# Optimization experiments

Measured on AMD Instinct MI355X. Metric: run time of the kernel, lower is better.

The kernel has to match this reference:

```python
import jax, jax.numpy as jnp
import numpy as np


def setup_inputs() -> dict:
    key = jax.random.key(0)
    k1, _ = jax.random.split(key)
    N, H, CH, T = 4, 8, 64, 2048
    qkv = jax.random.normal(k1, (N, H * 3 * CH, T), dtype=jnp.float32)
    rescale = jnp.ones((1,), dtype=jnp.float32)
    return {"qkv": qkv, "rescale": rescale, "n_heads": H}


def reference(qkv, rescale, n_heads):
    bs, width, length = qkv.shape
    ch = width // (3 * n_heads)
    # [N, H*3*C, T] -> [N*H, 3*C, T] -> three [N*H, C, T]
    qkv_h = qkv.reshape(bs * n_heads, 3 * ch, length)
    q, k, v = qkv_h[:, :ch], qkv_h[:, ch:2 * ch], qkv_h[:, 2 * ch:]
    scale = 1.0 / jnp.sqrt(jnp.sqrt(jnp.float32(ch)))
    # scores: [B*H, T, S]
    weight = jnp.einsum('bct,bcs->bts', q * scale, k * scale)
    weight = jax.nn.softmax(weight.astype(jnp.float32) * rescale[0], axis=-1).astype(qkv.dtype)
    a = jnp.einsum('bts,bcs->bct', weight, v)  # [B*H, C, T]
    return a.reshape(bs, n_heads * ch, length)
```

## Files before the change

### kernel.cpp

```cpp
#include <hip/hip_runtime.h>
#include <stdint.h>

typedef _Float16 half8 __attribute__((ext_vector_type(8)));
typedef _Float16 half4 __attribute__((ext_vector_type(4)));
typedef __fp16   fp16x2 __attribute__((ext_vector_type(2)));
typedef float    floatx4 __attribute__((ext_vector_type(4)));

#define T_LEN 2048
#define CH 64
#define BH 32
#define QTILE 64
#define LDP 72
#define PTP 72
#define FRAG_BH 131072

__global__ __launch_bounds__(256, 2)
void prep_kernel(const float* __restrict__ qkv, const float* __restrict__ rescale,
                 _Float16* __restrict__ ws)
{
    __shared__ _Float16 Qs[64][LDP];
    __shared__ _Float16 Ks[64][LDP];
    __shared__ _Float16 Vs[64][LDP];

    const int tid  = threadIdx.x;
    const int bh   = blockIdx.y;
    const int tile = blockIdx.x;
    const int x0   = tile * 64;

    const float qscale = 0.125f * 1.4426950408889634f * rescale[0];

    const float* qp = qkv + (size_t)(bh >> 3) * (1536 * T_LEN)
                          + (size_t)(bh & 7) * (192 * T_LEN);
    const float* kp = qp + 64 * T_LEN;
    const float* vp = qp + 128 * T_LEN;

    {
        const int a4 = (tid & 15) * 4;
        const int c4 = (tid >> 4) * 4;
        float4 rq[4], rk[4];
#pragma unroll
        for (int i = 0; i < 4; ++i) {
            rq[i] = *(const float4*)(qp + (size_t)(c4 + i) * T_LEN + x0 + a4);
            rk[i] = *(const float4*)(kp + (size_t)(c4 + i) * T_LEN + x0 + a4);
        }
#pragma unroll
        for (int j = 0; j < 4; ++j) {
            half4 hq, hk;
#pragma unroll
            for (int i = 0; i < 4; ++i) {
                hq[i] = (_Float16)((&rq[i].x)[j] * qscale);
                hk[i] = (_Float16)((&rk[i].x)[j]);
            }
            *(half4*)&Qs[a4 + j][c4] = hq;
            *(half4*)&Ks[a4 + j][c4] = hk;
        }
        const int s4 = (tid & 15) * 4;
        const int cv = tid >> 4;
#pragma unroll
        for (int i = 0; i < 4; ++i) {
            const int c = cv + 16 * i;
            float4 r = *(const float4*)(vp + (size_t)c * T_LEN + x0 + s4);
            half4 h; h[0]=(_Float16)r.x; h[1]=(_Float16)r.y; h[2]=(_Float16)r.z; h[3]=(_Float16)r.w;
            *(half4*)&Vs[c][s4] = h;
        }
    }
    __syncthreads();

    const int lane = tid & 63, wave = tid >> 6;
    const int l15 = lane & 15, quad = lane >> 4;
    _Float16* qf = ws;
    _Float16* kf = ws + (size_t)BH * FRAG_BH;
    _Float16* vf = ws + (size_t)2 * BH * FRAG_BH;

#pragma unroll
    for (int ks = 0; ks < 2; ++ks) {
        half8 hq = *(const half8*)&Qs[wave * 16 + l15][ks * 32 + quad * 8];
        half8 hk = *(const half8*)&Ks[wave * 16 + l15][ks * 32 + quad * 8];
        half8 hv = *(const half8*)&Vs[wave * 16 + l15][ks * 32 + quad * 8];
        const size_t gqk = (((size_t)bh * 128 + tile * 4 + wave) * 2 + ks) * 512 + lane * 8;
        *(half8*)(qf + gqk) = hq;
        *(half8*)(kf + gqk) = hk;
        *(half8*)(vf + (((size_t)bh * 32 + tile) * 8 + wave * 2 + ks) * 512 + lane * 8) = hv;
    }
}

__global__ __launch_bounds__(256, 4)
void attn_kernel(const _Float16* __restrict__ ws, float* __restrict__ out)
{
    __shared__ _Float16 Pt[4][16][PTP];

    const int tid  = threadIdx.x;
    const int wave = tid >> 6;
    const int lane = tid & 63;
    const int l15  = lane & 15;
    const int quad = lane >> 4;

    const int bid  = blockIdx.x;
    const int xcd  = bid & 7;
    const int slot = bid >> 3;
    const int bh   = (slot & 3) * 8 + xcd;
    const int tile = slot >> 2;
    const int t0   = tile * QTILE;

    const _Float16* qf = ws;
    const _Float16* kf = ws + (size_t)BH * FRAG_BH;
    const _Float16* vf = ws + (size_t)2 * BH * FRAG_BH;
    float* op = out + (size_t)bh * (CH * T_LEN);

    const _Float16* kfp = kf + (size_t)bh * FRAG_BH + lane * 8;
    const _Float16* vfp = vf + (size_t)bh * FRAG_BH + lane * 8;

    half8 bq[2];
#pragma unroll
    for (int ks = 0; ks < 2; ++ks)
        bq[ks] = *(const half8*)(qf +
            (((size_t)bh * 128 + tile * 4 + wave) * 2 + ks) * 512 + lane * 8);

    const floatx4 fzero = {0.f, 0.f, 0.f, 0.f};
    floatx4 oacc[4];
#pragma unroll
    for (int ct = 0; ct < 4; ++ct) oacc[ct] = fzero;
    floatx4 lacc = fzero;

    half8 bones;
#pragma unroll
    for (int i = 0; i < 8; ++i) bones[i] = (_Float16)1.0f;

    half8 ak[4][2];
    half8 bv[4][2];
    half8 ap[2];

    auto do_qk_exp = [&]() {
        floatx4 sacc[4];
#pragma unroll
        for (int mt = 0; mt < 4; ++mt) sacc[mt] = fzero;
#pragma unroll
        for (int mt = 0; mt < 4; ++mt)
#pragma unroll
            for (int ks = 0; ks < 2; ++ks)
                sacc[mt] = __builtin_amdgcn_mfma_f32_16x16x32_f16(
                    ak[mt][ks], bq[ks], sacc[mt], 0, 0, 0);

#pragma unroll
        for (int mt = 0; mt < 4; ++mt) {
            fp16x2 p01 = __builtin_amdgcn_cvt_pkrtz(
                __builtin_amdgcn_exp2f(sacc[mt][0]),
                __builtin_amdgcn_exp2f(sacc[mt][1]));
            fp16x2 p23 = __builtin_amdgcn_cvt_pkrtz(
                __builtin_amdgcn_exp2f(sacc[mt][2]),
                __builtin_amdgcn_exp2f(sacc[mt][3]));
            half4 ph;
            ph[0] = (_Float16)p01[0]; ph[1] = (_Float16)p01[1];
            ph[2] = (_Float16)p23[0]; ph[3] = (_Float16)p23[1];
            *(half4*)&Pt[wave][l15][mt * 16 + quad * 4] = ph;
        }
#pragma unroll
        for (int ks = 0; ks < 2; ++ks)
            ap[ks] = *(const half8*)&Pt[wave][l15][ks * 32 + quad * 8];
    };

#pragma unroll
    for (int mt = 0; mt < 4; ++mt)
#pragma unroll
        for (int ks = 0; ks < 2; ++ks)
            ak[mt][ks] = *(const half8*)(kfp + (size_t)(mt * 2 + ks) * 512);
#pragma unroll
    for (int ct = 0; ct < 4; ++ct)
#pragma unroll
        for (int ks = 0; ks < 2; ++ks)
            bv[ct][ks] = *(const half8*)(vfp + (size_t)(ct * 2 + ks) * 512);
    do_qk_exp();
#pragma unroll
    for (int mt = 0; mt < 4; ++mt)
#pragma unroll
        for (int ks = 0; ks < 2; ++ks)
            ak[mt][ks] = *(const half8*)(kfp + 4096 + (size_t)(mt * 2 + ks) * 512);

#pragma unroll 2
    for (int st = 1; st < 32; ++st) {
#pragma unroll
        for (int ks = 0; ks < 2; ++ks)
            lacc = __builtin_amdgcn_mfma_f32_16x16x32_f16(ap[ks], bones, lacc, 0, 0, 0);
#pragma unroll
        for (int ct = 0; ct < 4; ++ct)
#pragma unroll
            for (int ks = 0; ks < 2; ++ks)
                oacc[ct] = __builtin_amdgcn_mfma_f32_16x16x32_f16(
                    ap[ks], bv[ct][ks], oacc[ct], 0, 0, 0);

        const _Float16* vcur = vfp + (size_t)st * 4096;
#pragma unroll
        for (int ct = 0; ct < 4; ++ct)
#pragma unroll
            for (int ks = 0; ks < 2; ++ks)
                bv[ct][ks] = *(const half8*)(vcur + (size_t)(ct * 2 + ks) * 512);

        do_qk_exp();

        if (st < 31) {
            const _Float16* kcur = kfp + (size_t)(st + 1) * 4096;
#pragma unroll
            for (int mt = 0; mt < 4; ++mt)
#pragma unroll
                for (int ks = 0; ks < 2; ++ks)
                    ak[mt][ks] = *(const half8*)(kcur + (size_t)(mt * 2 + ks) * 512);
        }
    }

#pragma unroll
    for (int ks = 0; ks < 2; ++ks)
        lacc = __builtin_amdgcn_mfma_f32_16x16x32_f16(ap[ks], bones, lacc, 0, 0, 0);
#pragma unroll
    for (int ct = 0; ct < 4; ++ct)
#pragma unroll
        for (int ks = 0; ks < 2; ++ks)
            oacc[ct] = __builtin_amdgcn_mfma_f32_16x16x32_f16(
                ap[ks], bv[ct][ks], oacc[ct], 0, 0, 0);

    {
        float linv[4];
#pragma unroll
        for (int r = 0; r < 4; ++r) linv[r] = 1.0f / lacc[r];
#pragma unroll
        for (int ct = 0; ct < 4; ++ct) {
            const int c = ct * 16 + l15;
            const int t = t0 + wave * 16 + quad * 4;
            float4 o;
#pragma unroll
            for (int r = 0; r < 4; ++r)
                (&o.x)[r] = oacc[ct][r] * linv[r];
            *(float4*)(op + (size_t)c * T_LEN + t) = o;
        }
    }
}

extern "C" void kernel_launch(void* const* d_in, const int* in_sizes, int n_in,
                              void* d_out, int out_size, void* d_ws, size_t ws_size,
                              hipStream_t stream) {
    const float* qkv     = (const float*)d_in[0];
    const float* rescale = (const float*)d_in[1];
    float* out = (float*)d_out;
    _Float16* ws = (_Float16*)d_ws;

    prep_kernel<<<dim3(32, BH), dim3(256), 0, stream>>>(qkv, rescale, ws);
    attn_kernel<<<dim3(T_LEN / QTILE * BH), dim3(256), 0, stream>>>(ws, out);
}
```

Before: 153.5 us.

## Split key range across waves, keep P in registers, reduce partial outputs via LDS

The attention kernel now gives each wave a quarter of the key positions for all 64 queries in the tile, instead of a separate 16-query slice. Score-tile exponentials are fed straight into 16x16x16 MFMAs as the B operand, which removes the LDS round-trip for P. Row sums are accumulated in scalar registers rather than through ones-MFMAs, and V is stored in a new fragment layout that matches the new operand shape. The price is a cross-wave reduction of the partial outputs through LDS with several barriers, more accumulator registers (occupancy lowered to 3 blocks), and twice as many smaller MFMAs for the PV product.

```diff
diff --git a/kernel.cpp b/kernel.cpp
--- a/kernel.cpp
+++ b/kernel.cpp
@@ -5,13 +5,13 @@
 typedef _Float16 half4 __attribute__((ext_vector_type(4)));
 typedef __fp16   fp16x2 __attribute__((ext_vector_type(2)));
 typedef float    floatx4 __attribute__((ext_vector_type(4)));
+typedef unsigned uintx2 __attribute__((ext_vector_type(2)));
 
 #define T_LEN 2048
 #define CH 64
 #define BH 32
 #define QTILE 64
 #define LDP 72
-#define PTP 72
 #define FRAG_BH 131072
 
 __global__ __launch_bounds__(256, 2)
@@ -76,18 +76,24 @@
     for (int ks = 0; ks < 2; ++ks) {
         half8 hq = *(const half8*)&Qs[wave * 16 + l15][ks * 32 + quad * 8];
         half8 hk = *(const half8*)&Ks[wave * 16 + l15][ks * 32 + quad * 8];
-        half8 hv = *(const half8*)&Vs[wave * 16 + l15][ks * 32 + quad * 8];
         const size_t gqk = (((size_t)bh * 128 + tile * 4 + wave) * 2 + ks) * 512 + lane * 8;
         *(half8*)(qf + gqk) = hq;
         *(half8*)(kf + gqk) = hk;
-        *(half8*)(vf + (((size_t)bh * 32 + tile) * 8 + wave * 2 + ks) * 512 + lane * 8) = hv;
+    }
+#pragma unroll
+    for (int ct = 0; ct < 4; ++ct) {
+        half4 hv = *(const half4*)&Vs[ct * 16 + l15][wave * 16 + quad * 4];
+        *(half4*)(vf + (size_t)bh * FRAG_BH
+                     + ((size_t)(tile * 4 + wave) * 4 + ct) * 256 + lane * 4) = hv;
     }
 }
 
-__global__ __launch_bounds__(256, 4)
+__global__ __launch_bounds__(256, 3)
 void attn_kernel(const _Float16* __restrict__ ws, float* __restrict__ out)
 {
-    __shared__ _Float16 Pt[4][16][PTP];
+    __shared__ float Os[4][64][16];
+    __shared__ float Lred[4][64];
+    __shared__ float Lfin[64];
 
     const int tid  = threadIdx.x;
     const int wave = tid >> 6;
@@ -107,129 +113,104 @@
     const _Float16* vf = ws + (size_t)2 * BH * FRAG_BH;
     float* op = out + (size_t)bh * (CH * T_LEN);
 
-    const _Float16* kfp = kf + (size_t)bh * FRAG_BH + lane * 8;
-    const _Float16* vfp = vf + (size_t)bh * FRAG_BH + lane * 8;
-
-    half8 bq[2];
-#pragma unroll
-    for (int ks = 0; ks < 2; ++ks)
-        bq[ks] = *(const half8*)(qf +
-            (((size_t)bh * 128 + tile * 4 + wave) * 2 + ks) * 512 + lane * 8);
+    const _Float16* kfp = kf + (size_t)bh * FRAG_BH + wave * 1024 + lane * 8;
+    const _Float16* vfp = vf + (size_t)bh * FRAG_BH + wave * 1024 + lane * 4;
+
+    half8 bq[4][2];
+#pragma unroll
+    for (int tt = 0; tt < 4; ++tt)
+#pragma unroll
+        for (int ks = 0; ks < 2; ++ks)
+            bq[tt][ks] = *(const half8*)(qf +
+                (((size_t)bh * 128 + tile * 4 + tt) * 2 + ks) * 512 + lane * 8);
 
     const floatx4 fzero = {0.f, 0.f, 0.f, 0.f};
-    floatx4 oacc[4];
-#pragma unroll
-    for (int ct = 0; ct < 4; ++ct) oacc[ct] = fzero;
-    floatx4 lacc = fzero;
-
-    half8 bones;
-#pragma unroll
-    for (int i = 0; i < 8; ++i) bones[i] = (_Float16)1.0f;
-
-    half8 ak[4][2];
-    half8 bv[4][2];
-    half8 ap[2];
-
-    auto do_qk_exp = [&]() {
-        floatx4 sacc[4];
-#pragma unroll
-        for (int mt = 0; mt < 4; ++mt) sacc[mt] = fzero;
-#pragma unroll
-        for (int mt = 0; mt < 4; ++mt)
+    floatx4 oacc[4][4];
+#pragma unroll
+    for (int ct = 0; ct < 4; ++ct)
+#pragma unroll
+        for (int tt = 0; tt < 4; ++tt) oacc[ct][tt] = fzero;
+    float lsum[4] = {0.f, 0.f, 0.f, 0.f};
+
+    half8 akA[2], akB[2];
+    half4 bvA[4], bvB[4];
+
+    auto load_kv = [&](half8 (&ak)[2], half4 (&bv)[4], int st) {
+        const _Float16* kp = kfp + (size_t)st * 4096;
+        ak[0] = *(const half8*)kp;
+        ak[1] = *(const half8*)(kp + 512);
+        const _Float16* vp = vfp + (size_t)st * 4096;
+#pragma unroll
+        for (int ct = 0; ct < 4; ++ct)
+            bv[ct] = *(const half4*)(vp + ct * 256);
+    };
+
+    auto body = [&](half8 (&akC)[2], half4 (&bvC)[4],
+                    half8 (&akN)[2], half4 (&bvN)[4], int st) {
+        if (st < 31) load_kv(akN, bvN, st + 1);
+#pragma unroll
+        for (int tt = 0; tt < 4; ++tt) {
+            floatx4 sacc = fzero;
 #pragma unroll
             for (int ks = 0; ks < 2; ++ks)
-                sacc[mt] = __builtin_amdgcn_mfma_f32_16x16x32_f16(
-                    ak[mt][ks], bq[ks], sacc[mt], 0, 0, 0);
-
-#pragma unroll
-        for (int mt = 0; mt < 4; ++mt) {
-            fp16x2 p01 = __builtin_amdgcn_cvt_pkrtz(
-                __builtin_amdgcn_exp2f(sacc[mt][0]),
-                __builtin_amdgcn_exp2f(sacc[mt][1]));
-            fp16x2 p23 = __builtin_amdgcn_cvt_pkrtz(
-                __builtin_amdgcn_exp2f(sacc[mt][2]),
-                __builtin_amdgcn_exp2f(sacc[mt][3]));
-            half4 ph;
-            ph[0] = (_Float16)p01[0]; ph[1] = (_Float16)p01[1];
-            ph[2] = (_Float16)p23[0]; ph[3] = (_Float16)p23[1];
-            *(half4*)&Pt[wave][l15][mt * 16 + quad * 4] = ph;
-        }
-#pragma unroll
-        for (int ks = 0; ks < 2; ++ks)
-            ap[ks] = *(const half8*)&Pt[wave][l15][ks * 32 + quad * 8];
+                sacc = __builtin_amdgcn_mfma_f32_16x16x32_f16(
+                    akC[ks], bq[tt][ks], sacc, 0, 0, 0);
+            float e0 = __builtin_amdgcn_exp2f(sacc[0]);
+            float e1 = __builtin_amdgcn_exp2f(sacc[1]);
+            float e2 = __builtin_amdgcn_exp2f(sacc[2]);
+            float e3 = __builtin_amdgcn_exp2f(sacc[3]);
+            lsum[tt] += (e0 + e1) + (e2 + e3);
+            fp16x2 p01 = __builtin_amdgcn_cvt_pkrtz(e0, e1);
+            fp16x2 p23 = __builtin_amdgcn_cvt_pkrtz(e2, e3);
+            uintx2 uu;
+            uu[0] = __builtin_bit_cast(unsigned, p01);
+            uu[1] = __builtin_bit_cast(unsigned, p23);
+            half4 pb = __builtin_bit_cast(half4, uu);
+#pragma unroll
+            for (int ct = 0; ct < 4; ++ct)
+                oacc[ct][tt] = __builtin_amdgcn_mfma_f32_16x16x16f16(
+                    bvC[ct], pb, oacc[ct][tt], 0, 0, 0);
+        }
     };
 
-#pragma unroll
-    for (int mt = 0; mt < 4; ++mt)
-#pragma unroll
-        for (int ks = 0; ks < 2; ++ks)
-            ak[mt][ks] = *(const half8*)(kfp + (size_t)(mt * 2 + ks) * 512);
-#pragma unroll
-    for (int ct = 0; ct < 4; ++ct)
-#pragma unroll
-        for (int ks = 0; ks < 2; ++ks)
-            bv[ct][ks] = *(const half8*)(vfp + (size_t)(ct * 2 + ks) * 512);
-    do_qk_exp();
-#pragma unroll
-    for (int mt = 0; mt < 4; ++mt)
-#pragma unroll
-        for (int ks = 0; ks < 2; ++ks)
-            ak[mt][ks] = *(const half8*)(kfp + 4096 + (size_t)(mt * 2 + ks) * 512);
-
-#pragma unroll 2
-    for (int st = 1; st < 32; ++st) {
-#pragma unroll
-        for (int ks = 0; ks < 2; ++ks)
-            lacc = __builtin_amdgcn_mfma_f32_16x16x32_f16(ap[ks], bones, lacc, 0, 0, 0);
-#pragma unroll
-        for (int ct = 0; ct < 4; ++ct)
-#pragma unroll
-            for (int ks = 0; ks < 2; ++ks)
-                oacc[ct] = __builtin_amdgcn_mfma_f32_16x16x32_f16(
-                    ap[ks], bv[ct][ks], oacc[ct], 0, 0, 0);
-
-        const _Float16* vcur = vfp + (size_t)st * 4096;
-#pragma unroll
-        for (int ct = 0; ct < 4; ++ct)
-#pragma unroll
-            for (int ks = 0; ks < 2; ++ks)
-                bv[ct][ks] = *(const half8*)(vcur + (size_t)(ct * 2 + ks) * 512);
-
-        do_qk_exp();
-
-        if (st < 31) {
-            const _Float16* kcur = kfp + (size_t)(st + 1) * 4096;
-#pragma unroll
-            for (int mt = 0; mt < 4; ++mt)
-#pragma unroll
-                for (int ks = 0; ks < 2; ++ks)
-                    ak[mt][ks] = *(const half8*)(kcur + (size_t)(mt * 2 + ks) * 512);
-        }
-    }
-
-#pragma unroll
-    for (int ks = 0; ks < 2; ++ks)
-        lacc = __builtin_amdgcn_mfma_f32_16x16x32_f16(ap[ks], bones, lacc, 0, 0, 0);
-#pragma unroll
-    for (int ct = 0; ct < 4; ++ct)
-#pragma unroll
-        for (int ks = 0; ks < 2; ++ks)
-            oacc[ct] = __builtin_amdgcn_mfma_f32_16x16x32_f16(
-                ap[ks], bv[ct][ks], oacc[ct], 0, 0, 0);
-
-    {
-        float linv[4];
-#pragma unroll
-        for (int r = 0; r < 4; ++r) linv[r] = 1.0f / lacc[r];
-#pragma unroll
-        for (int ct = 0; ct < 4; ++ct) {
-            const int c = ct * 16 + l15;
-            const int t = t0 + wave * 16 + quad * 4;
-            float4 o;
-#pragma unroll
-            for (int r = 0; r < 4; ++r)
-                (&o.x)[r] = oacc[ct][r] * linv[r];
-            *(float4*)(op + (size_t)c * T_LEN + t) = o;
+    load_kv(akA, bvA, 0);
+    for (int st = 0; st < 32; st += 2) {
+        body(akA, bvA, akB, bvB, st);
+        body(akB, bvB, akA, bvA, st + 1);
+    }
+
+#pragma unroll
+    for (int tt = 0; tt < 4; ++tt) {
+        float v = lsum[tt];
+        v += __shfl_xor(v, 16, 64);
+        v += __shfl_xor(v, 32, 64);
+        lsum[tt] = v;
+    }
+    if (quad == 0) {
+#pragma unroll
+        for (int tt = 0; tt < 4; ++tt) Lred[wave][tt * 16 + l15] = lsum[tt];
+    }
+    __syncthreads();
+    if (tid < 64)
+        Lfin[tid] = (Lred[0][tid] + Lred[1][tid]) + (Lred[2][tid] + Lred[3][tid]);
+
+    for (int ct = 0; ct < 4; ++ct) {
+        __syncthreads();
+#pragma unroll
+        for (int tt = 0; tt < 4; ++tt)
+            *(floatx4*)&Os[wave][tt * 16 + l15][quad * 4] = oacc[ct][tt];
+        __syncthreads();
+        const int t  = tid & 63;
+        const int c4 = (tid >> 6) * 4;
+        float4 s0 = *(const float4*)&Os[0][t][c4];
+        float4 s1 = *(const float4*)&Os[1][t][c4];
+        float4 s2 = *(const float4*)&Os[2][t][c4];
+        float4 s3 = *(const float4*)&Os[3][t][c4];
+        const float inv = 1.0f / Lfin[t];
+#pragma unroll
+        for (int j = 0; j < 4; ++j) {
+            float v = (((&s0.x)[j] + (&s1.x)[j]) + ((&s2.x)[j] + (&s3.x)[j])) * inv;
+            op[(size_t)(ct * 16 + c4 + j) * T_LEN + t0 + t] = v;
         }
     }
 }
```

New measurement: 136.5 us. 11.1% less time.
